# Kernel optimization log

Hardware: AMD Instinct MI355X
Metric: run time of the kernel (lower is better)

The kernel has to match this reference:

```python
import math
import numpy as np
import jax
import jax.numpy as jnp

B_IN, B_L1, B_L2 = 10, 6, 3
BATCH, NUM_POINTS = 4, 512
F1, F2, F_OUT = 8, 16, 10
NB = BATCH * NUM_POINTS
N_GRID_S2, N_GRID_SO3 = 24, 144


def _lf(n):
    return math.lgamma(n + 1)


def wigner_d(l, beta):
    """Wigner small-d matrices d^l_{m',m}(beta). beta: np [K] -> [K, 2l+1, 2l+1]."""
    beta = np.asarray(beta, dtype=np.float64)
    K = beta.shape[0]
    d = np.zeros((K, 2 * l + 1, 2 * l + 1))
    c, s = np.cos(beta / 2.0), np.sin(beta / 2.0)
    for mi, mp in enumerate(range(-l, l + 1)):
        for ni, m in enumerate(range(-l, l + 1)):
            k0, k1 = max(0, m - mp), min(l + m, l - mp)
            acc = np.zeros(K)
            for k in range(k0, k1 + 1):
                lg = 0.5 * (_lf(l + mp) + _lf(l - mp) + _lf(l + m) + _lf(l - m)) - _lf(l + m - k) - _lf(k) - _lf(mp - m + k) - _lf(l - mp - k)
                acc = acc + ((-1.0) ** (mp - m + k)) * np.exp(lg) * c ** (2 * l - 2 * k + m - mp) * s ** (mp - m + 2 * k)
            d[:, mi, ni] = acc
    return d


def quad_beta_weights(b):
    """Driscoll-Healy quadrature betas and weights at bandwidth b."""
    k = np.arange(2 * b)
    beta = np.pi * (2 * k + 1) / (4 * b)
    j = np.arange(b)[:, None]
    w = (2.0 / b) * np.sin(beta) * np.sum(np.sin((2 * j + 1) * beta[None, :]) / (2 * j + 1), axis=0)
    return beta, w


# near-identity kernel grids (as in s2cnn): s2 grid 3 betas x 8 alphas, so3 grid x 6 gammas
_b = np.arange(1, 4) * (np.pi / 8) / 3
_a = np.linspace(0, 2 * np.pi, 8, endpoint=False)
_GB1, _GA1 = [g.ravel() for g in np.meshgrid(_b, _a, indexing='ij')]
_g = np.linspace(0, 2 * np.pi, 6, endpoint=False)
_GB2, _GA2, _GG2 = [g.ravel() for g in np.meshgrid(_b, _a, _g, indexing='ij')]

_BETA_IN, _W_IN = quad_beta_weights(B_IN)
_BETA_L1, _W_L1 = quad_beta_weights(B_L1)
_BETA_L2, _W_L2 = quad_beta_weights(B_L2)

# S2 FFT tables: quadrature-weighted d^l_{m,0}(beta_k), l < b_l1
_S2FFT_D = [jnp.asarray((wigner_d(l, _BETA_IN)[:, :, l] * _W_IN[:, None]).astype(np.complex64)) for l in range(B_L1)]
# S2 kernel basis psi1[l]: [24, 2l+1] = d^l_{m,0}(beta_g) e^{-i m alpha_g}
_PSI1 = []
for l in range(B_L1):
    m = np.arange(-l, l + 1)
    _PSI1.append(jnp.asarray((wigner_d(l, _GB1)[:, :, l] * np.exp(-1j * m[None, :] * _GA1[:, None])).astype(np.complex64)))
# SO3 inverse-FFT d matrices at b_l1 quadrature betas
_D_L1 = [jnp.asarray(wigner_d(l, _BETA_L1).astype(np.complex64)) for l in range(B_L1)]
# SO3 FFT tables at b_l1 (output bandwidth b_l2)
_SO3FFT_D = [jnp.asarray((wigner_d(l, _BETA_L1) * _W_L1[:, None, None]).astype(np.complex64)) for l in range(B_L2)]
# SO3 kernel basis psi2[l]: [144, 2l+1, 2l+1] = e^{-i m a} d^l_{mn}(b) e^{-i n g}
_PSI2 = []
for l in range(B_L2):
    m = np.arange(-l, l + 1)
    ph = np.exp(-1j * m[None, :, None] * _GA2[:, None, None]) * np.exp(-1j * m[None, None, :] * _GG2[:, None, None])
    _PSI2.append(jnp.asarray((wigner_d(l, _GB2) * ph).astype(np.complex64)))
_D_L2 = [jnp.asarray(wigner_d(l, _BETA_L2).astype(np.complex64)) for l in range(B_L2)]
_W_INT = jnp.asarray(_W_L2.astype(np.float32))


def s2_fft(x, b_out):
    # x: [n, f, 2b(beta), 2b(alpha)] real -> list_l of [n, f, 2l+1] complex
    two_b = x.shape[-1]
    F = jnp.fft.fft(x, axis=-1)
    out = []
    for l in range(b_out):
        idx = np.arange(-l, l + 1) % two_b
        out.append(jnp.einsum('nfkm,km->nfm', F[..., idx], _S2FFT_D[l]))
    return out


def so3_ifft_list(z, b_out, d_list):
    # z[l]: [n, fo, 2l+1(m), 2l+1(p)] -> real [n, fo, 2b(beta), 2b(alpha), 2b(gamma)]
    n2 = 2 * b_out
    n, fo = z[0].shape[:2]
    Fh = jnp.zeros((n, fo, n2, n2, n2), jnp.complex64)
    for l in range(b_out):
        idx = np.arange(-l, l + 1) % n2
        blk = (2 * l + 1) * jnp.einsum('nomp,kmp->nokmp', z[l], d_list[l])
        Fh = Fh.at[:, :, :, idx[:, None], idx[None, :]].add(blk)
    return jnp.real(jnp.fft.ifft2(Fh, axes=(-2, -1)) * (n2 * n2))


def s2_conv(x, w, bias):
    xs = s2_fft(x, B_L1)
    wc = w.astype(jnp.complex64)
    z = []
    for l in range(B_L1):
        y = jnp.einsum('iog,gm->iom', wc, _PSI1[l])  # kernel spectrum [fi, fo, 2l+1]
        z.append(jnp.einsum('nim,iop->nomp', xs[l], jnp.conj(y)))
    return so3_ifft_list(z, B_L1, _D_L1) + bias[None, :, None, None, None]


def so3_fft(x, b_out):
    # x: [n, f, 2b(beta), 2b(alpha), 2b(gamma)] -> list_l of [n, f, 2l+1, 2l+1]
    two_b = x.shape[-1]
    F = jnp.fft.fft2(x, axes=(-2, -1))
    out = []
    for l in range(b_out):
        idx = np.arange(-l, l + 1) % two_b
        out.append(jnp.einsum('nfkmp,kmp->nfmp', F[:, :, :, idx[:, None], idx[None, :]], _SO3FFT_D[l]))
    return out


def so3_conv(x, w, bias):
    xs = so3_fft(x, B_L2)
    wc = w.astype(jnp.complex64)
    z = []
    for l in range(B_L2):
        y = jnp.einsum('iog,gmp->iomp', wc, _PSI2[l])  # [fi, fo, 2l+1, 2l+1]
        z.append(jnp.einsum('nimk,iopk->nomp', xs[l], jnp.conj(y)))
    return so3_ifft_list(z, B_L2, _D_L2) + bias[None, :, None, None, None]


def so3_integrate(x):
    # mean over alpha, gamma; quadrature-weighted sum over beta
    return jnp.einsum('nfk,k->nf', x.mean(axis=(-2, -1)), _W_INT)


def forward(x, w1, b1, w2, b2, w_out, bias_out):
    h = jax.nn.relu(s2_conv(x, w1, b1))
    h = jax.nn.relu(so3_conv(h, w2, b2))
    feat = so3_integrate(h).reshape(BATCH, NUM_POINTS, F2).transpose(0, 2, 1)  # [B, F2, P]
    pooled = feat.max(axis=-1)  # MaxPool1d(kernel_size=num_points) + squeeze
    return pooled @ w_out.T + bias_out


def setup_inputs():
    ks = jax.random.split(jax.random.key(0), 4)
    return {
        'x': jax.random.normal(ks[0], (NB, 1, 2 * B_IN, 2 * B_IN), jnp.float32),
        'w1': jax.random.normal(ks[1], (1, F1, N_GRID_S2), jnp.float32) * 0.1,
        'b1': jnp.zeros((F1,), jnp.float32),
        'w2': jax.random.normal(ks[2], (F1, F2, N_GRID_SO3), jnp.float32) * 0.05,
        'b2': jnp.zeros((F2,), jnp.float32),
        'w_out': jax.random.normal(ks[3], (F_OUT, F2), jnp.float32) * 0.1,
        'bias_out': jnp.zeros((F_OUT,), jnp.float32),
    }


def reference(x, w1, b1, w2, b2, w_out, bias_out):
    return forward(x, w1, b1, w2, b2, w_out, bias_out)
```

## Files before the change

### kernel.cpp

```cpp
#include <hip/hip_runtime.h>
#include <cmath>

typedef float2 c32;

__device__ __forceinline__ void cmadd(c32& acc, c32 a, float cr, float ci){
    acc.x += a.x*cr - a.y*ci;
    acc.y += a.x*ci + a.y*cr;
}

__host__ __device__ constexpr int M12(int x){ return ((x%12)+12)%12; }
__host__ __device__ constexpr int M6(int x){ return ((x%6)+6)%6; }

#define SQ32 0.86602540378443864676f
#define RT22 0.70710678118654752440f
static constexpr float CW12[12] = {1.f, SQ32, 0.5f, 0.f, -0.5f, -SQ32, -1.f, -SQ32, -0.5f, 0.f, 0.5f, SQ32};
static constexpr float SW12[12] = {0.f, 0.5f, SQ32, 1.f, SQ32, 0.5f, 0.f, -0.5f, -SQ32, -1.f, -SQ32, -0.5f};
static constexpr float CW6[6] = {1.f, 0.5f, -0.5f, -1.f, -0.5f, 0.5f};
static constexpr float SW6[6] = {0.f, SQ32, SQ32, 0.f, -SQ32, -SQ32};
static constexpr float CW8[8] = {1.f, RT22, 0.f, -RT22, -1.f, -RT22, 0.f, RT22};
static constexpr float SW8[8] = {0.f, RT22, 1.f, RT22, 0.f, -RT22, -1.f, -RT22};
static constexpr float CW20_[6] = {1.f, 0.95105651629515357212f, 0.80901699437494742410f,
                                   0.58778525229247312917f, 0.30901699437494742410f, 0.f};
static constexpr float SW20_[6] = {0.f, 0.30901699437494742410f, 0.58778525229247312917f,
                                   0.80901699437494742410f, 0.95105651629515357212f, 1.f};

#define O_CY1  0
#define O_CY2P 528
#define O_XS   (O_CY2P + 14080)
#define O_XS2P (O_XS + 73728)
#define N_C32_TOTAL (O_XS2P + 2048*8*30)

#define O_S2D  0
#define O_D1S  1752
#define O_DG   (O_D1S + 6336)
#define O_D2P  (O_DG + 360)
#define O_POOLP (O_D2P + 360)

#define DPI 3.14159265358979323846

__device__ __forceinline__ void cell_decode(int c, int& L, int& m, int& p){
    int base;
    if (c < 1){ L=0; base=0; } else if (c < 6){ L=1; base=1; }
    else if (c < 15){ L=2; base=6; } else if (c < 28){ L=3; base=15; }
    else if (c < 45){ L=4; base=28; } else { L=5; base=45; }
    int r = c - base;
    if (r < 2*L){ m = r>>1; p = (r&1)? L : -L; }
    else { m = L; p = (r - 2*L) - L; }
}

static constexpr double FCT[13] = {1.,1.,2.,6.,24.,120.,720.,5040.,40320.,
                                   362880.,3628800.,39916800.,479001600.};

__device__ __forceinline__ double dipow(double b, int e){
    double r = 1.0;
    while (e){ if (e & 1) r *= b; b *= b; e >>= 1; }
    return r;
}

__device__ double dev_wig(int l, int mp, int m, double beta){
    int k0 = max(0, m - mp), k1 = min(l + m, l - mp);
    double c = cos(0.5*beta), s = sin(0.5*beta);
    double fnum = sqrt(FCT[l+mp]*FCT[l-mp]*FCT[l+m]*FCT[l-m]);
    double acc = 0.0;
    for (int k = k0; k <= k1; ++k){
        double t = fnum / (FCT[l+m-k]*FCT[k]*FCT[mp-m+k]*FCT[l-mp-k])
                 * dipow(c, 2*l-2*k+m-mp) * dipow(s, mp-m+2*k);
        acc += ((mp-m+k) & 1) ? -t : t;
    }
    return acc;
}

__device__ double dev_qw(int b, double beta){
    double s = 0.0;
    for (int j = 0; j < b; ++j) s += sin((2.0*j+1.0)*beta)/(2.0*j+1.0);
    return (2.0/b)*sin(beta)*s;
}

__global__ __launch_bounds__(256) void k_setup(c32* cb, float* fb,
                                               const float* __restrict__ w1,
                                               const float* __restrict__ w2){
    __shared__ float wsh[144];
    __shared__ float s_d2sg[225];
    __shared__ c32 W1s[3][8][5];
    __shared__ c32 Rs[3][5][5];
    int bid = blockIdx.x, tid = threadIdx.x;
    if (bid < 128){
        int o = bid >> 3, i = bid & 7;
        for (int c = tid; c < 144; c += 256) wsh[c] = w2[(i*16+o)*144 + c];
        for (int c = tid; c < 225; c += 256){
            int qi = c%5; int t = c/5; int pi = t%5; t /= 5; int ib = t%3; int l = t/3;
            float v = 0.f;
            if (pi < 2*l+1 && qi < 2*l+1){ double beta = (ib+1)*DPI/24.0; v = (float)dev_wig(l, pi-l, qi-l, beta); }
            s_d2sg[c] = v;
        }
        __syncthreads();
        for (int c = tid; c < 120; c += 256){
            int ib = c/40, r = c%40, ia = r/5, qi = r%5;
            int q = qi - 2; int qm = ((q%6)+6)%6;
            float wr = CW6[qm], wi = SW6[qm];
            float er = 1.f, ei = 0.f, sx = 0.f, sy = 0.f;
            const float* wrow = wsh + ib*48 + ia*6;
            #pragma unroll
            for (int ig = 0; ig < 6; ++ig){
                float w = wrow[ig];
                sx += w*er; sy += w*ei;
                float nr = er*wr - ei*wi; ei = er*wi + ei*wr; er = nr;
            }
            W1s[ib][ia][qi] = make_float2(sx, sy);
        }
        __syncthreads();
        for (int c = tid; c < 75; c += 256){
            int ib = c/25, r = c%25, pi = r/5, qi = r%5;
            int p = pi - 2; int pm = ((p%8)+8)%8;
            float wr = CW8[pm], wi = SW8[pm];
            float er = 1.f, ei = 0.f;
            c32 acc = make_float2(0.f,0.f);
            #pragma unroll
            for (int ia = 0; ia < 8; ++ia){
                c32 wv = W1s[ib][ia][qi];
                acc.x += wv.x*er - wv.y*ei;
                acc.y += wv.x*ei + wv.y*er;
                float nr = er*wr - ei*wi; ei = er*wi + ei*wr; er = nr;
            }
            Rs[ib][pi][qi] = acc;
        }
        __syncthreads();
        for (int c = tid; c < 110; c += 256){
            int cell = c/5, qt = c%5;
            int l, p;
            if (cell == 0){ l=0; p=0; }
            else if (cell < 7){ l=1; p=(cell-1)%3 - 1; }
            else { l=2; p=(cell-7)%5 - 2; }
            c32 acc = make_float2(0.f,0.f);
            if (qt < 2*l+1){
                int q = qt - l;
                #pragma unroll
                for (int ib = 0; ib < 3; ++ib){
                    float d = s_d2sg[(l*3+ib)*25 + (p+l)*5 + (q+l)];
                    c32 rv = Rs[ib][p+2][q+2];
                    acc.x += d*rv.x; acc.y += d*rv.y;
                }
            }
            cb[O_CY2P + ((o*22+cell)*8 + i)*5 + qt] = acc;
        }
        return;
    }
    int gid = (bid-128)*256 + tid;
    if (gid < 1320){
        int mi = gid%11; int t = gid/11; int k = t%20; int l = t/20;
        float v = 0.f;
        if (mi < 2*l+1){
            double beta = DPI*(2*k+1)/40.0;
            v = (float)(dev_wig(l, mi-l, 0, beta) * dev_qw(10, beta));
        }
        fb[O_S2D+gid] = v; return;
    }
    gid -= 1320;
    if (gid < 528){
        int pi = gid%11; int t = gid/11; int l = t%6; int o = t/6;
        c32 acc = make_float2(0.f,0.f);
        if (pi < 2*l+1){
            int p = pi - l;
            int pm = ((p%8)+8)%8;
            float wr = CW8[pm], wi = SW8[pm];
            for (int ib = 0; ib < 3; ++ib){
                float d = (float)dev_wig(l, pi-l, 0, (ib+1)*DPI/24.0);
                float er = 1.f, ei = 0.f, sx = 0.f, sy = 0.f;
                #pragma unroll
                for (int ia = 0; ia < 8; ++ia){
                    float w = w1[o*24 + ib*8 + ia];
                    sx += w*er; sy += w*ei;
                    float nr = er*wr - ei*wi; ei = er*wi + ei*wr; er = nr;
                }
                acc.x += d*sx; acc.y += d*sy;
            }
        }
        cb[O_CY1 + (o*6+l)*11 + pi] = acc;
        return;
    }
    gid -= 528;
    if (gid < 6336){
        int k = gid%12; int t = gid/12; int l = t%8; int cell = t/8;
        int L, m, p; cell_decode(cell, L, m, p);
        float v = 0.f;
        if (l < 6 && l >= L){
            double beta = DPI*(2*k+1)/24.0;
            v = (float)dev_wig(l, m, p, beta);
        }
        fb[O_D1S+gid] = v; return;
    }
    gid -= 6336;
    if (gid < 360){
        int k = gid%12; int slot = gid/12;
        int lm = slot/5, qt = slot%5;
        int l = lm==0?0:(lm<3?1:2);
        int m = lm==0?0:(lm<3?lm-1:lm-3);
        float v = 0.f;
        if (qt < 2*l+1){
            double beta = DPI*(2*k+1)/24.0;
            v = (float)(dev_wig(l, m, qt-l, beta) * dev_qw(6, beta));
        }
        fb[O_DG+gid] = v; return;
    }
    gid -= 360;
    if (gid < 360){
        int lp = gid%4; int t = gid/4; int k = t%6; int cell = t/6;
        int m = cell/5, pi = cell%5, p = pi-2, ap = p<0?-p:p;
        float v = 0.f;
        if (lp < 3 && lp >= m && lp >= ap){
            double beta = DPI*(2*k+1)/12.0;
            v = (float)dev_wig(lp, m, p, beta);
        }
        fb[O_D2P+gid] = v; return;
    }
}

__global__ __launch_bounds__(256) void k_s2fft(const float* __restrict__ x, const float* __restrict__ fb,
                                               c32* __restrict__ XS){
    __shared__ float xsh[1600];
    __shared__ c32 F1[4][20][6];
    int n0 = blockIdx.x*4, tid = threadIdx.x;
    for (int i = tid; i < 1600; i += 256) xsh[i] = x[n0*400 + i];
    __syncthreads();
    for (int i = tid; i < 480; i += 256){
        int nl = i/120, r = i - nl*120, k = r/6, m = r - k*6;
        float wr = CW20_[m], wi = -SW20_[m];
        float er = 1.f, ei = 0.f, ax = 0.f, ay = 0.f;
        const float* row = xsh + nl*400 + k*20;
        #pragma unroll
        for (int a = 0; a < 20; ++a){
            float v = row[a];
            ax += v*er; ay += v*ei;
            float nr = er*wr - ei*wi; ei = er*wi + ei*wr; er = nr;
        }
        F1[nl][k][m] = make_float2(ax, ay);
    }
    __syncthreads();
    if (tid < 144){
        int nl = tid/36, t = tid - nl*36;
        int l = 0; while ((l+1)*(l+1) <= t) ++l;
        int mi = t - l*l; int m = mi - l;
        c32 acc = make_float2(0.f,0.f);
        for (int k = 0; k < 20; ++k){
            float d = fb[O_S2D + (l*20+k)*11 + mi];
            c32 F = (m >= 0) ? F1[nl][k][m] : make_float2(F1[nl][k][-m].x, -F1[nl][k][-m].y);
            acc.x += d*F.x; acc.y += d*F.y;
        }
        XS[(n0+nl)*36 + t] = acc;
    }
}

__global__ __launch_bounds__(256) void k_layer1(const c32* __restrict__ cb, const float* __restrict__ fb,
                                                const float* __restrict__ b1, c32* __restrict__ xs2p){
    __shared__ c32 xs_sh[36];
    __shared__ c32 u1[936];
    __shared__ c32 u2[936];
    __shared__ c32 Gg[468];
    __shared__ c32 Gs[180];
    int tid = threadIdx.x;
    int n = blockIdx.x >> 3, o = blockIdx.x & 7;
    float bias = b1[o];
    if (tid < 36) xs_sh[tid] = cb[O_XS + n*36 + tid];
    __syncthreads();

    for (int c = tid; c < 396; c += 256){
        int l = c/66, mp = c - l*66, m = mp/11, pi = mp - m*11;
        int p = pi - 5, ap = p < 0 ? -p : p;
        c32 v = make_float2(0.f, 0.f);
        if (m <= l && ap <= l){
            c32 a = xs_sh[l*l + l + m];
            c32 b = cb[O_CY1 + o*66 + l*11 + p + l];
            float f = (float)(2*l+1);
            v.x = f*(a.x*b.x - a.y*b.y); v.y = f*(a.x*b.y + a.y*b.x);
        }
        u1[c] = v;
    }
    __syncthreads();

    if (tid < 132){
        int cell = tid >> 1, kh = tid & 1;
        int L, m, p; cell_decode(cell, L, m, p);
        int mp = m*11 + p + 5;
        c32 acc[6];
        #pragma unroll
        for (int j = 0; j < 6; ++j) acc[j] = make_float2(0.f,0.f);
        for (int l = L; l < 6; ++l){
            c32 z = u1[l*66 + mp];
            const float* dp = fb + O_D1S + (cell*8 + l)*12 + kh*6;
            #pragma unroll
            for (int j = 0; j < 6; ++j){
                float d = dp[j];
                acc[j].x += d*z.x; acc[j].y += d*z.y;
            }
        }
        #pragma unroll
        for (int j = 0; j < 6; ++j) u2[mp*13 + kh*6 + j] = acc[j];
    }
    __syncthreads();

    if (tid < 72){
        int m = tid/12, k = tid - m*12;
        c32 S0 = u2[(m*11+5)*13 + k];
        c32 E[5], O[5];
        #pragma unroll
        for (int p = 1; p <= 5; ++p){
            c32 a = u2[(m*11+5+p)*13 + k], b = u2[(m*11+5-p)*13 + k];
            E[p-1] = make_float2(a.x+b.x, a.y+b.y);
            O[p-1] = make_float2(a.x-b.x, a.y-b.y);
        }
        #pragma unroll
        for (int g = 0; g < 6; ++g){
            float vex=0.f, vey=0.f, vox=0.f, voy=0.f;
            #pragma unroll
            for (int p = 1; p <= 5; ++p){
                const float cc = CW12[M12(p*g)], ss = SW12[M12(p*g)];
                float vx = E[p-1].x*cc - O[p-1].y*ss;
                float vy = E[p-1].y*cc + O[p-1].x*ss;
                if (p & 1){ vox += vx; voy += vy; } else { vex += vx; vey += vy; }
            }
            float tex = S0.x + vex, tey = S0.y + vey;
            u1[(m*12+g)*13 + k]   = make_float2(tex + vox, tey + voy);
            u1[(m*12+g+6)*13 + k] = make_float2(tex - vox, tey - voy);
        }
    }
    __syncthreads();

    float* hh = (float*)u2;
    if (tid < 144){
        int g = tid/12, k = tid - g*12;
        c32 t1 = u1[(1*12+g)*13+k], t2 = u1[(2*12+g)*13+k], t3 = u1[(3*12+g)*13+k];
        c32 t4 = u1[(4*12+g)*13+k], t5 = u1[(5*12+g)*13+k];
        float base = u1[(0*12+g)*13+k].x + bias;
        #pragma unroll
        for (int a = 0; a < 6; ++a){
            float od = t1.x*CW12[M12(1*a)] - t1.y*SW12[M12(1*a)]
                     + t3.x*CW12[M12(3*a)] - t3.y*SW12[M12(3*a)]
                     + t5.x*CW12[M12(5*a)] - t5.y*SW12[M12(5*a)];
            float ev = t2.x*CW12[M12(2*a)] - t2.y*SW12[M12(2*a)]
                     + t4.x*CW12[M12(4*a)] - t4.y*SW12[M12(4*a)];
            float h0 = base + 2.f*(ev+od);
            float h1 = base + 2.f*(ev-od);
            hh[(g*12+a)*13+k]     = h0 > 0.f ? h0 : 0.f;
            hh[(g*12+a+6)*13+k]   = h1 > 0.f ? h1 : 0.f;
        }
    }
    __syncthreads();

    if (tid < 144){
        int a = tid/12, k = tid - a*12;
        float hv[12];
        #pragma unroll
        for (int g = 0; g < 12; ++g) hv[g] = hh[(g*12+a)*13+k];
        float s0 = 0.f;
        #pragma unroll
        for (int g = 0; g < 12; ++g) s0 += hv[g];
        Gg[a*13+k] = make_float2(s0, 0.f);
        #pragma unroll
        for (int mg = 1; mg < 3; ++mg){
            float ax = 0.f, ay = 0.f;
            #pragma unroll
            for (int g = 0; g < 12; ++g){
                const int tt = M12(mg*g);
                ax += hv[g]*CW12[tt]; ay -= hv[g]*SW12[tt];
            }
            Gg[(mg*12+a)*13+k] = make_float2(ax, ay);
        }
    }
    __syncthreads();

    if (tid < 108){
        int j = tid/36, rr = tid - j*36, mg = rr/12, k = rr - mg*12;
        const c32* gp = Gg + mg*156 + k;
        if (j == 0){
            float sx = 0.f, sy = 0.f;
            #pragma unroll
            for (int a = 0; a < 6; ++a){
                c32 xa = gp[a*13], ya = gp[(a+6)*13];
                sx += xa.x + ya.x; sy += xa.y + ya.y;
            }
            Gs[(2*3+mg)*12+k] = make_float2(sx, sy);
        } else if (j == 1){
            float Cx=0.f,Cy=0.f,Sx=0.f,Sy=0.f;
            #pragma unroll
            for (int a = 0; a < 6; ++a){
                c32 xa = gp[a*13], ya = gp[(a+6)*13];
                float ux = xa.x - ya.x, uy = xa.y - ya.y;
                const float cc = CW12[a], ss = SW12[a];
                Cx += ux*cc; Cy += uy*cc;
                Sx += ux*ss; Sy += uy*ss;
            }
            Gs[(3*3+mg)*12+k] = make_float2(Cx + Sy, Cy - Sx);
            Gs[(1*3+mg)*12+k] = make_float2(Cx - Sy, Cy + Sx);
        } else {
            float Cx=0.f,Cy=0.f,Sx=0.f,Sy=0.f;
            #pragma unroll
            for (int a = 0; a < 6; ++a){
                c32 xa = gp[a*13], ya = gp[(a+6)*13];
                float ux = xa.x + ya.x, uy = xa.y + ya.y;
                const float cc = CW12[M12(2*a)], ss = SW12[M12(2*a)];
                Cx += ux*cc; Cy += uy*cc;
                Sx += ux*ss; Sy += uy*ss;
            }
            Gs[(4*3+mg)*12+k] = make_float2(Cx + Sy, Cy - Sx);
            Gs[(0*3+mg)*12+k] = make_float2(Cx - Sy, Cy + Sx);
        }
    }
    __syncthreads();

    if (tid < 30){
        int lm = tid/5, qt = tid - lm*5;
        int l = lm==0?0:(lm<3?1:2);
        int m = lm==0?0:(lm<3?lm-1:lm-3);
        c32 acc = make_float2(0.f,0.f);
        if (qt < 2*l+1){
            int q = qt - l;
            #pragma unroll
            for (int k = 0; k < 12; ++k){
                float d = fb[O_DG + tid*12 + k];
                c32 gvv;
                if (q >= 0) gvv = Gs[((m+2)*3 + q)*12 + k];
                else { c32 w = Gs[((2-m)*3 + (-q))*12 + k]; gvv = make_float2(w.x, -w.y); }
                acc.x += d*gvv.x; acc.y += d*gvv.y;
            }
        }
        xs2p[(n*8+o)*30 + tid] = acc;
    }
}

__global__ __launch_bounds__(256) void k_layer2(const c32* __restrict__ cb, const float* __restrict__ fb,
                                                const float* __restrict__ b2, float* __restrict__ poolp){
    __shared__ c32 xs2sh[960];
    __shared__ c32 zp2[4][384];
    __shared__ c32 T2[1728];
    __shared__ float part[576];
    __shared__ float wint_sh[6];
    int tid = threadIdx.x, n0 = blockIdx.x*4;
    for (int c = tid; c < 960; c += 256) xs2sh[c] = cb[O_XS2P + n0*240 + c];
    if (tid < 6){ double beta = DPI*(2*tid+1)/12.0; wint_sh[tid] = (float)dev_qw(3, beta); }
    __syncthreads();

    for (int c = tid; c < 352; c += 256){
        int o = c/22, cell = c - o*22;
        int l, lm;
        if (cell == 0){ l=0; lm=0; }
        else if (cell < 7){ l=1; lm=1+(cell-1)/3; }
        else { l=2; lm=3+(cell-7)/5; }
        const c32* cy = cb + O_CY2P + (o*22+cell)*40;
        c32 acc[4];
        #pragma unroll
        for (int nl = 0; nl < 4; ++nl) acc[nl] = make_float2(0.f,0.f);
        #pragma unroll
        for (int i = 0; i < 8; ++i){
            #pragma unroll
            for (int qt = 0; qt < 5; ++qt){
                c32 yv = cy[i*5+qt];
                #pragma unroll
                for (int nl = 0; nl < 4; ++nl){
                    c32 xv = xs2sh[nl*240 + (i*6+lm)*5 + qt];
                    acc[nl].x += xv.x*yv.x - xv.y*yv.y;
                    acc[nl].y += xv.x*yv.y + xv.y*yv.x;
                }
            }
        }
        float f = (float)(2*l+1);
        #pragma unroll
        for (int nl = 0; nl < 4; ++nl)
            zp2[nl][o*24+cell] = make_float2(f*acc[nl].x, f*acc[nl].y);
    }
    __syncthreads();

    float runmax = -3.4e38f;
    for (int nl = 0; nl < 4; ++nl){
        for (int c = tid; c < 288; c += 256){
            int o = c/18, r = c - o*18, k = r/3, m = r - k*3;
            c32 s2v[5];
            #pragma unroll
            for (int pi = 0; pi < 5; ++pi){
                const int p = pi-2; const int ap = p<0?-p:p;
                c32 acc = make_float2(0.f,0.f);
                #pragma unroll
                for (int l = 0; l < 3; ++l){
                    if (l >= ap){
                        float d = fb[O_D2P + ((m*5+pi)*6+k)*4 + l];
                        int cell = (l==0) ? 0 : ((l==1) ? 1+m*3+(p+1) : 7+m*5+(p+2));
                        c32 z = zp2[nl][o*24+cell];
                        acc.x += d*z.x; acc.y += d*z.y;
                    }
                }
                s2v[pi] = acc;
            }
            #pragma unroll
            for (int g = 0; g < 6; ++g){
                c32 t = make_float2(0.f,0.f);
                #pragma unroll
                for (int pi = 0; pi < 5; ++pi){
                    const int tt = M6((pi-2)*g);
                    cmadd(t, s2v[pi], CW6[tt], SW6[tt]);
                }
                T2[((o*6+k)*3+m)*6+g] = t;
            }
        }
        __syncthreads();
        for (int c = tid; c < 576; c += 256){
            int o = c/36, r = c - o*36, k = r/6, g = r - k*6;
            c32 t0 = T2[((o*6+k)*3+0)*6+g];
            c32 t1 = T2[((o*6+k)*3+1)*6+g];
            c32 t2 = T2[((o*6+k)*3+2)*6+g];
            float base = t0.x + b2[o];
            float s = 0.f;
            #pragma unroll
            for (int a = 0; a < 6; ++a){
                float h = base + 2.f*(t1.x*CW6[M6(a)]   - t1.y*SW6[M6(a)])
                               + 2.f*(t2.x*CW6[M6(2*a)] - t2.y*SW6[M6(2*a)]);
                s += h > 0.f ? h : 0.f;
            }
            part[c] = s * wint_sh[k];
        }
        __syncthreads();
        if (tid < 16){
            float s = 0.f;
            #pragma unroll
            for (int j = 0; j < 36; ++j) s += part[tid*36+j];
            runmax = fmaxf(runmax, s * (1.f/36.f));
        }
        __syncthreads();
    }
    if (tid < 16) poolp[blockIdx.x*16 + tid] = runmax;
}

__global__ __launch_bounds__(256) void k_head(const float* __restrict__ poolp,
                                              const float* __restrict__ w_out,
                                              const float* __restrict__ bias_out,
                                              float* __restrict__ out){
    __shared__ float red[256];
    __shared__ float pool_s[64];
    int tid = threadIdx.x;
    int pair = tid >> 2, q = tid & 3;
    int b = pair >> 4, o = pair & 15;
    float m = -3.4e38f;
    for (int j = q; j < 128; j += 4)
        m = fmaxf(m, poolp[(b*128 + j)*16 + o]);
    red[tid] = m;
    __syncthreads();
    if (tid < 64)
        pool_s[tid] = fmaxf(fmaxf(red[tid*4], red[tid*4+1]),
                            fmaxf(red[tid*4+2], red[tid*4+3]));
    __syncthreads();
    if (tid < 40){
        int bb = tid/10, jj = tid%10;
        float s = bias_out[jj];
        #pragma unroll
        for (int oo = 0; oo < 16; ++oo) s += pool_s[bb*16+oo]*w_out[jj*16+oo];
        out[tid] = s;
    }
}

extern "C" void kernel_launch(void* const* d_in, const int* in_sizes, int n_in,
                              void* d_out, int out_size, void* d_ws, size_t ws_size,
                              hipStream_t stream){
    const float* x        = (const float*)d_in[0];
    const float* w1       = (const float*)d_in[1];
    const float* b1       = (const float*)d_in[2];
    const float* w2       = (const float*)d_in[3];
    const float* b2       = (const float*)d_in[4];
    const float* w_out    = (const float*)d_in[5];
    const float* bias_out = (const float*)d_in[6];
    float* out = (float*)d_out;

    c32*   cb = (c32*)d_ws;
    float* fb = (float*)(cb + N_C32_TOTAL);

    k_setup<<<163, 256, 0, stream>>>(cb, fb, w1, w2);
    k_s2fft<<<512, 256, 0, stream>>>(x, fb, cb + O_XS);
    k_layer1<<<2048*8, 256, 0, stream>>>(cb, fb, b1, cb + O_XS2P);
    k_layer2<<<512, 256, 0, stream>>>(cb, fb, b2, fb + O_POOLP);
    k_head<<<1, 256, 0, stream>>>(fb + O_POOLP, w_out, bias_out, out);
}
```

Before: 172.9 us.

## Fuse all stages into one persistent cooperative kernel with grid syncs

Merges the S2 FFT, layer-1, layer-2 and head kernels into a single persistent cooperative kernel. Blocks loop over work units and use grid-wide syncs between stages, and shared memory is reused through one aliased buffer. Layer 2 now handles one point per unit instead of four, so the reuse of each CY2P load across points is lost. Per-point features are written out and then pooled in a final stage. The change removes launch overhead and inter-kernel gaps, at the cost of grid-sync overhead and occupancy limited to co-resident blocks.

```diff
diff --git a/kernel.cpp b/kernel.cpp
--- a/kernel.cpp
+++ b/kernel.cpp
@@ -1,5 +1,8 @@
 #include <hip/hip_runtime.h>
+#include <hip/hip_cooperative_groups.h>
 #include <cmath>
+
+namespace cg = cooperative_groups;
 
 typedef float2 c32;
 
@@ -34,7 +37,8 @@
 #define O_D1S  1752
 #define O_DG   (O_D1S + 6336)
 #define O_D2P  (O_DG + 360)
-#define O_POOLP (O_D2P + 360)
+#define O_WINT (O_D2P + 360)
+#define O_FEAT (O_WINT + 8)
 
 #define DPI 3.14159265358979323846
 
@@ -213,345 +217,358 @@
         }
         fb[O_D2P+gid] = v; return;
     }
-}
-
-__global__ __launch_bounds__(256) void k_s2fft(const float* __restrict__ x, const float* __restrict__ fb,
-                                               c32* __restrict__ XS){
-    __shared__ float xsh[1600];
-    __shared__ c32 F1[4][20][6];
-    int n0 = blockIdx.x*4, tid = threadIdx.x;
-    for (int i = tid; i < 1600; i += 256) xsh[i] = x[n0*400 + i];
-    __syncthreads();
-    for (int i = tid; i < 480; i += 256){
-        int nl = i/120, r = i - nl*120, k = r/6, m = r - k*6;
-        float wr = CW20_[m], wi = -SW20_[m];
-        float er = 1.f, ei = 0.f, ax = 0.f, ay = 0.f;
-        const float* row = xsh + nl*400 + k*20;
-        #pragma unroll
-        for (int a = 0; a < 20; ++a){
-            float v = row[a];
-            ax += v*er; ay += v*ei;
-            float nr = er*wr - ei*wi; ei = er*wi + ei*wr; er = nr;
-        }
-        F1[nl][k][m] = make_float2(ax, ay);
-    }
-    __syncthreads();
-    if (tid < 144){
-        int nl = tid/36, t = tid - nl*36;
-        int l = 0; while ((l+1)*(l+1) <= t) ++l;
-        int mi = t - l*l; int m = mi - l;
-        c32 acc = make_float2(0.f,0.f);
-        for (int k = 0; k < 20; ++k){
-            float d = fb[O_S2D + (l*20+k)*11 + mi];
-            c32 F = (m >= 0) ? F1[nl][k][m] : make_float2(F1[nl][k][-m].x, -F1[nl][k][-m].y);
-            acc.x += d*F.x; acc.y += d*F.y;
-        }
-        XS[(n0+nl)*36 + t] = acc;
-    }
-}
-
-__global__ __launch_bounds__(256) void k_layer1(const c32* __restrict__ cb, const float* __restrict__ fb,
-                                                const float* __restrict__ b1, c32* __restrict__ xs2p){
-    __shared__ c32 xs_sh[36];
-    __shared__ c32 u1[936];
-    __shared__ c32 u2[936];
-    __shared__ c32 Gg[468];
-    __shared__ c32 Gs[180];
+    gid -= 360;
+    if (gid < 6){
+        double beta = DPI*(2*gid+1)/12.0;
+        fb[O_WINT+gid] = (float)dev_qw(3, beta); return;
+    }
+}
+
+__global__ __launch_bounds__(256) void k_fused(const float* __restrict__ x,
+                                               c32* __restrict__ cb,
+                                               const float* __restrict__ fb,
+                                               const float* __restrict__ b1,
+                                               const float* __restrict__ b2,
+                                               const float* __restrict__ w_out,
+                                               const float* __restrict__ bias_out,
+                                               float* __restrict__ feat,
+                                               float* __restrict__ out){
+    __shared__ c32 U[2556];
+    cg::grid_group grid = cg::this_grid();
     int tid = threadIdx.x;
-    int n = blockIdx.x >> 3, o = blockIdx.x & 7;
-    float bias = b1[o];
-    if (tid < 36) xs_sh[tid] = cb[O_XS + n*36 + tid];
-    __syncthreads();
-
-    for (int c = tid; c < 396; c += 256){
-        int l = c/66, mp = c - l*66, m = mp/11, pi = mp - m*11;
-        int p = pi - 5, ap = p < 0 ? -p : p;
-        c32 v = make_float2(0.f, 0.f);
-        if (m <= l && ap <= l){
-            c32 a = xs_sh[l*l + l + m];
-            c32 b = cb[O_CY1 + o*66 + l*11 + p + l];
-            float f = (float)(2*l+1);
-            v.x = f*(a.x*b.x - a.y*b.y); v.y = f*(a.x*b.y + a.y*b.x);
-        }
-        u1[c] = v;
-    }
-    __syncthreads();
-
-    if (tid < 132){
-        int cell = tid >> 1, kh = tid & 1;
-        int L, m, p; cell_decode(cell, L, m, p);
-        int mp = m*11 + p + 5;
-        c32 acc[6];
-        #pragma unroll
-        for (int j = 0; j < 6; ++j) acc[j] = make_float2(0.f,0.f);
-        for (int l = L; l < 6; ++l){
-            c32 z = u1[l*66 + mp];
-            const float* dp = fb + O_D1S + (cell*8 + l)*12 + kh*6;
+    int nblk = gridDim.x;
+
+    {
+        float* xsh = (float*)U;
+        c32* F1 = U + 800;
+        for (int u = blockIdx.x; u < 512; u += nblk){
+            int n0 = u*4;
+            for (int i = tid; i < 1600; i += 256) xsh[i] = x[n0*400 + i];
+            __syncthreads();
+            for (int i = tid; i < 480; i += 256){
+                int nl = i/120, r = i - nl*120, k = r/6, m = r - k*6;
+                float wr = CW20_[m], wi = -SW20_[m];
+                float er = 1.f, ei = 0.f, ax = 0.f, ay = 0.f;
+                const float* row = xsh + nl*400 + k*20;
+                #pragma unroll
+                for (int a = 0; a < 20; ++a){
+                    float v = row[a];
+                    ax += v*er; ay += v*ei;
+                    float nr = er*wr - ei*wi; ei = er*wi + ei*wr; er = nr;
+                }
+                F1[(nl*20+k)*6+m] = make_float2(ax, ay);
+            }
+            __syncthreads();
+            if (tid < 144){
+                int nl = tid/36, t = tid - nl*36;
+                int l = 0; while ((l+1)*(l+1) <= t) ++l;
+                int mi = t - l*l; int m = mi - l;
+                c32 acc = make_float2(0.f,0.f);
+                for (int k = 0; k < 20; ++k){
+                    float d = fb[O_S2D + (l*20+k)*11 + mi];
+                    c32 F = (m >= 0) ? F1[(nl*20+k)*6+m]
+                                     : make_float2(F1[(nl*20+k)*6-m].x, -F1[(nl*20+k)*6-m].y);
+                    acc.x += d*F.x; acc.y += d*F.y;
+                }
+                cb[O_XS + (n0+nl)*36 + t] = acc;
+            }
+            __syncthreads();
+        }
+    }
+    grid.sync();
+
+    {
+        c32* u1 = U;
+        c32* u2 = U + 936;
+        c32* Gg = U + 1872;
+        c32* Gs = U + 2340;
+        c32* xs_sh = U + 2520;
+        float* hh = (float*)u2;
+        for (int u = blockIdx.x; u < 16384; u += nblk){
+            int n = u >> 3, o = u & 7;
+            float bias = b1[o];
+            if (tid < 36) xs_sh[tid] = cb[O_XS + n*36 + tid];
+            __syncthreads();
+
+            for (int c = tid; c < 396; c += 256){
+                int l = c/66, mp = c - l*66, m = mp/11, pi = mp - m*11;
+                int p = pi - 5, ap = p < 0 ? -p : p;
+                c32 v = make_float2(0.f, 0.f);
+                if (m <= l && ap <= l){
+                    c32 a = xs_sh[l*l + l + m];
+                    c32 b = cb[O_CY1 + o*66 + l*11 + p + l];
+                    float f = (float)(2*l+1);
+                    v.x = f*(a.x*b.x - a.y*b.y); v.y = f*(a.x*b.y + a.y*b.x);
+                }
+                u1[c] = v;
+            }
+            __syncthreads();
+
+            if (tid < 132){
+                int cell = tid >> 1, kh = tid & 1;
+                int L, m, p; cell_decode(cell, L, m, p);
+                int mp = m*11 + p + 5;
+                c32 acc[6];
+                #pragma unroll
+                for (int j = 0; j < 6; ++j) acc[j] = make_float2(0.f,0.f);
+                for (int l = L; l < 6; ++l){
+                    c32 z = u1[l*66 + mp];
+                    const float* dp = fb + O_D1S + (cell*8 + l)*12 + kh*6;
+                    #pragma unroll
+                    for (int j = 0; j < 6; ++j){
+                        float d = dp[j];
+                        acc[j].x += d*z.x; acc[j].y += d*z.y;
+                    }
+                }
+                #pragma unroll
+                for (int j = 0; j < 6; ++j) u2[mp*13 + kh*6 + j] = acc[j];
+            }
+            __syncthreads();
+
+            if (tid < 72){
+                int m = tid/12, k = tid - m*12;
+                c32 S0 = u2[(m*11+5)*13 + k];
+                c32 E[5], O[5];
+                #pragma unroll
+                for (int p = 1; p <= 5; ++p){
+                    c32 a = u2[(m*11+5+p)*13 + k], b = u2[(m*11+5-p)*13 + k];
+                    E[p-1] = make_float2(a.x+b.x, a.y+b.y);
+                    O[p-1] = make_float2(a.x-b.x, a.y-b.y);
+                }
+                #pragma unroll
+                for (int g = 0; g < 6; ++g){
+                    float vex=0.f, vey=0.f, vox=0.f, voy=0.f;
+                    #pragma unroll
+                    for (int p = 1; p <= 5; ++p){
+                        const float cc = CW12[M12(p*g)], ss = SW12[M12(p*g)];
+                        float vx = E[p-1].x*cc - O[p-1].y*ss;
+                        float vy = E[p-1].y*cc + O[p-1].x*ss;
+                        if (p & 1){ vox += vx; voy += vy; } else { vex += vx; vey += vy; }
+                    }
+                    float tex = S0.x + vex, tey = S0.y + vey;
+                    u1[(m*12+g)*13 + k]   = make_float2(tex + vox, tey + voy);
+                    u1[(m*12+g+6)*13 + k] = make_float2(tex - vox, tey - voy);
+                }
+            }
+            __syncthreads();
+
+            if (tid < 144){
+                int g = tid/12, k = tid - g*12;
+                c32 t1 = u1[(1*12+g)*13+k], t2 = u1[(2*12+g)*13+k], t3 = u1[(3*12+g)*13+k];
+                c32 t4 = u1[(4*12+g)*13+k], t5 = u1[(5*12+g)*13+k];
+                float base = u1[(0*12+g)*13+k].x + bias;
+                #pragma unroll
+                for (int a = 0; a < 6; ++a){
+                    float od = t1.x*CW12[M12(1*a)] - t1.y*SW12[M12(1*a)]
+                             + t3.x*CW12[M12(3*a)] - t3.y*SW12[M12(3*a)]
+                             + t5.x*CW12[M12(5*a)] - t5.y*SW12[M12(5*a)];
+                    float ev = t2.x*CW12[M12(2*a)] - t2.y*SW12[M12(2*a)]
+                             + t4.x*CW12[M12(4*a)] - t4.y*SW12[M12(4*a)];
+                    float h0 = base + 2.f*(ev+od);
+                    float h1 = base + 2.f*(ev-od);
+                    hh[(g*12+a)*13+k]     = h0 > 0.f ? h0 : 0.f;
+                    hh[(g*12+a+6)*13+k]   = h1 > 0.f ? h1 : 0.f;
+                }
+            }
+            __syncthreads();
+
+            if (tid < 144){
+                int a = tid/12, k = tid - a*12;
+                float hv[12];
+                #pragma unroll
+                for (int g = 0; g < 12; ++g) hv[g] = hh[(g*12+a)*13+k];
+                float s0 = 0.f;
+                #pragma unroll
+                for (int g = 0; g < 12; ++g) s0 += hv[g];
+                Gg[a*13+k] = make_float2(s0, 0.f);
+                #pragma unroll
+                for (int mg = 1; mg < 3; ++mg){
+                    float ax = 0.f, ay = 0.f;
+                    #pragma unroll
+                    for (int g = 0; g < 12; ++g){
+                        const int tt = M12(mg*g);
+                        ax += hv[g]*CW12[tt]; ay -= hv[g]*SW12[tt];
+                    }
+                    Gg[(mg*12+a)*13+k] = make_float2(ax, ay);
+                }
+            }
+            __syncthreads();
+
+            if (tid < 108){
+                int j = tid/36, rr = tid - j*36, mg = rr/12, k = rr - mg*12;
+                const c32* gp = Gg + mg*156 + k;
+                if (j == 0){
+                    float sx = 0.f, sy = 0.f;
+                    #pragma unroll
+                    for (int a = 0; a < 6; ++a){
+                        c32 xa = gp[a*13], ya = gp[(a+6)*13];
+                        sx += xa.x + ya.x; sy += xa.y + ya.y;
+                    }
+                    Gs[(2*3+mg)*12+k] = make_float2(sx, sy);
+                } else if (j == 1){
+                    float Cx=0.f,Cy=0.f,Sx=0.f,Sy=0.f;
+                    #pragma unroll
+                    for (int a = 0; a < 6; ++a){
+                        c32 xa = gp[a*13], ya = gp[(a+6)*13];
+                        float ux = xa.x - ya.x, uy = xa.y - ya.y;
+                        const float cc = CW12[a], ss = SW12[a];
+                        Cx += ux*cc; Cy += uy*cc;
+                        Sx += ux*ss; Sy += uy*ss;
+                    }
+                    Gs[(3*3+mg)*12+k] = make_float2(Cx + Sy, Cy - Sx);
+                    Gs[(1*3+mg)*12+k] = make_float2(Cx - Sy, Cy + Sx);
+                } else {
+                    float Cx=0.f,Cy=0.f,Sx=0.f,Sy=0.f;
+                    #pragma unroll
+                    for (int a = 0; a < 6; ++a){
+                        c32 xa = gp[a*13], ya = gp[(a+6)*13];
+                        float ux = xa.x + ya.x, uy = xa.y + ya.y;
+                        const float cc = CW12[M12(2*a)], ss = SW12[M12(2*a)];
+                        Cx += ux*cc; Cy += uy*cc;
+                        Sx += ux*ss; Sy += uy*ss;
+                    }
+                    Gs[(4*3+mg)*12+k] = make_float2(Cx + Sy, Cy - Sx);
+                    Gs[(0*3+mg)*12+k] = make_float2(Cx - Sy, Cy + Sx);
+                }
+            }
+            __syncthreads();
+
+            if (tid < 30){
+                int lm = tid/5, qt = tid - lm*5;
+                int l = lm==0?0:(lm<3?1:2);
+                int m = lm==0?0:(lm<3?lm-1:lm-3);
+                c32 acc = make_float2(0.f,0.f);
+                if (qt < 2*l+1){
+                    int q = qt - l;
+                    #pragma unroll
+                    for (int k = 0; k < 12; ++k){
+                        float d = fb[O_DG + tid*12 + k];
+                        c32 gvv;
+                        if (q >= 0) gvv = Gs[((m+2)*3 + q)*12 + k];
+                        else { c32 w = Gs[((2-m)*3 + (-q))*12 + k]; gvv = make_float2(w.x, -w.y); }
+                        acc.x += d*gvv.x; acc.y += d*gvv.y;
+                    }
+                }
+                cb[O_XS2P + (n*8+o)*30 + tid] = acc;
+            }
+            __syncthreads();
+        }
+    }
+    grid.sync();
+
+    {
+        c32* xs2sh = U;
+        c32* zp2   = U + 240;
+        c32* T2    = U + 624;
+        float* part = (float*)U;
+        float* wint_sh = (float*)(U + 2530);
+        for (int u = blockIdx.x; u < 2048; u += nblk){
+            if (tid < 240) xs2sh[tid] = cb[O_XS2P + u*240 + tid];
+            if (tid >= 248 && tid < 254) wint_sh[tid-248] = fb[O_WINT + tid-248];
+            __syncthreads();
+
+            for (int c = tid; c < 352; c += 256){
+                int o = c/22, cell = c - o*22;
+                int l, lm;
+                if (cell == 0){ l=0; lm=0; }
+                else if (cell < 7){ l=1; lm=1+(cell-1)/3; }
+                else { l=2; lm=3+(cell-7)/5; }
+                const c32* cy = cb + O_CY2P + (o*22+cell)*40;
+                c32 acc = make_float2(0.f,0.f);
+                #pragma unroll
+                for (int i = 0; i < 8; ++i){
+                    #pragma unroll
+                    for (int qt = 0; qt < 5; ++qt){
+                        c32 xv = xs2sh[(i*6+lm)*5 + qt];
+                        c32 yv = cy[i*5+qt];
+                        acc.x += xv.x*yv.x - xv.y*yv.y;
+                        acc.y += xv.x*yv.y + xv.y*yv.x;
+                    }
+                }
+                float f = (float)(2*l+1);
+                zp2[o*24+cell] = make_float2(f*acc.x, f*acc.y);
+            }
+            __syncthreads();
+
+            for (int c = tid; c < 288; c += 256){
+                int o = c/18, r = c - o*18, k = r/3, m = r - k*3;
+                c32 s2v[5];
+                #pragma unroll
+                for (int pi = 0; pi < 5; ++pi){
+                    const int p = pi-2; const int ap = p<0?-p:p;
+                    c32 acc = make_float2(0.f,0.f);
+                    #pragma unroll
+                    for (int l = 0; l < 3; ++l){
+                        if (l >= ap){
+                            float d = fb[O_D2P + ((m*5+pi)*6+k)*4 + l];
+                            int cell = (l==0) ? 0 : ((l==1) ? 1+m*3+(p+1) : 7+m*5+(p+2));
+                            c32 z = zp2[o*24+cell];
+                            acc.x += d*z.x; acc.y += d*z.y;
+                        }
+                    }
+                    s2v[pi] = acc;
+                }
+                #pragma unroll
+                for (int g = 0; g < 6; ++g){
+                    c32 t = make_float2(0.f,0.f);
+                    #pragma unroll
+                    for (int pi = 0; pi < 5; ++pi){
+                        const int tt = M6((pi-2)*g);
+                        cmadd(t, s2v[pi], CW6[tt], SW6[tt]);
+                    }
+                    T2[((o*6+k)*3+m)*6+g] = t;
+                }
+            }
+            __syncthreads();
+
+            for (int c = tid; c < 576; c += 256){
+                int o = c/36, r = c - o*36, k = r/6, g = r - k*6;
+                c32 t0 = T2[((o*6+k)*3+0)*6+g];
+                c32 t1 = T2[((o*6+k)*3+1)*6+g];
+                c32 t2 = T2[((o*6+k)*3+2)*6+g];
+                float base = t0.x + b2[o];
+                float s = 0.f;
+                #pragma unroll
+                for (int a = 0; a < 6; ++a){
+                    float h = base + 2.f*(t1.x*CW6[M6(a)]   - t1.y*SW6[M6(a)])
+                                   + 2.f*(t2.x*CW6[M6(2*a)] - t2.y*SW6[M6(2*a)]);
+                    s += h > 0.f ? h : 0.f;
+                }
+                part[c] = s * wint_sh[k];
+            }
+            __syncthreads();
+            if (tid < 16){
+                float s = 0.f;
+                #pragma unroll
+                for (int j = 0; j < 36; ++j) s += part[tid*36+j];
+                feat[u*16+tid] = s * (1.f/36.f);
+            }
+            __syncthreads();
+        }
+    }
+    grid.sync();
+
+    if (blockIdx.x == 0){
+        float* red = (float*)U;
+        float* pool_s = (float*)(U + 128);
+        int pair = tid >> 2, q = tid & 3;
+        int b = pair >> 4, o = pair & 15;
+        float m = -3.4e38f;
+        for (int j = q; j < 512; j += 4)
+            m = fmaxf(m, feat[(b*512+j)*16 + o]);
+        red[tid] = m;
+        __syncthreads();
+        if (tid < 64)
+            pool_s[tid] = fmaxf(fmaxf(red[tid*4], red[tid*4+1]),
+                                fmaxf(red[tid*4+2], red[tid*4+3]));
+        __syncthreads();
+        if (tid < 40){
+            int bb = tid/10, jj = tid%10;
+            float s = bias_out[jj];
             #pragma unroll
-            for (int j = 0; j < 6; ++j){
-                float d = dp[j];
-                acc[j].x += d*z.x; acc[j].y += d*z.y;
-            }
-        }
-        #pragma unroll
-        for (int j = 0; j < 6; ++j) u2[mp*13 + kh*6 + j] = acc[j];
-    }
-    __syncthreads();
-
-    if (tid < 72){
-        int m = tid/12, k = tid - m*12;
-        c32 S0 = u2[(m*11+5)*13 + k];
-        c32 E[5], O[5];
-        #pragma unroll
-        for (int p = 1; p <= 5; ++p){
-            c32 a = u2[(m*11+5+p)*13 + k], b = u2[(m*11+5-p)*13 + k];
-            E[p-1] = make_float2(a.x+b.x, a.y+b.y);
-            O[p-1] = make_float2(a.x-b.x, a.y-b.y);
-        }
-        #pragma unroll
-        for (int g = 0; g < 6; ++g){
-            float vex=0.f, vey=0.f, vox=0.f, voy=0.f;
-            #pragma unroll
-            for (int p = 1; p <= 5; ++p){
-                const float cc = CW12[M12(p*g)], ss = SW12[M12(p*g)];
-                float vx = E[p-1].x*cc - O[p-1].y*ss;
-                float vy = E[p-1].y*cc + O[p-1].x*ss;
-                if (p & 1){ vox += vx; voy += vy; } else { vex += vx; vey += vy; }
-            }
-            float tex = S0.x + vex, tey = S0.y + vey;
-            u1[(m*12+g)*13 + k]   = make_float2(tex + vox, tey + voy);
-            u1[(m*12+g+6)*13 + k] = make_float2(tex - vox, tey - voy);
-        }
-    }
-    __syncthreads();
-
-    float* hh = (float*)u2;
-    if (tid < 144){
-        int g = tid/12, k = tid - g*12;
-        c32 t1 = u1[(1*12+g)*13+k], t2 = u1[(2*12+g)*13+k], t3 = u1[(3*12+g)*13+k];
-        c32 t4 = u1[(4*12+g)*13+k], t5 = u1[(5*12+g)*13+k];
-        float base = u1[(0*12+g)*13+k].x + bias;
-        #pragma unroll
-        for (int a = 0; a < 6; ++a){
-            float od = t1.x*CW12[M12(1*a)] - t1.y*SW12[M12(1*a)]
-                     + t3.x*CW12[M12(3*a)] - t3.y*SW12[M12(3*a)]
-                     + t5.x*CW12[M12(5*a)] - t5.y*SW12[M12(5*a)];
-            float ev = t2.x*CW12[M12(2*a)] - t2.y*SW12[M12(2*a)]
-                     + t4.x*CW12[M12(4*a)] - t4.y*SW12[M12(4*a)];
-            float h0 = base + 2.f*(ev+od);
-            float h1 = base + 2.f*(ev-od);
-            hh[(g*12+a)*13+k]     = h0 > 0.f ? h0 : 0.f;
-            hh[(g*12+a+6)*13+k]   = h1 > 0.f ? h1 : 0.f;
-        }
-    }
-    __syncthreads();
-
-    if (tid < 144){
-        int a = tid/12, k = tid - a*12;
-        float hv[12];
-        #pragma unroll
-        for (int g = 0; g < 12; ++g) hv[g] = hh[(g*12+a)*13+k];
-        float s0 = 0.f;
-        #pragma unroll
-        for (int g = 0; g < 12; ++g) s0 += hv[g];
-        Gg[a*13+k] = make_float2(s0, 0.f);
-        #pragma unroll
-        for (int mg = 1; mg < 3; ++mg){
-            float ax = 0.f, ay = 0.f;
-            #pragma unroll
-            for (int g = 0; g < 12; ++g){
-                const int tt = M12(mg*g);
-                ax += hv[g]*CW12[tt]; ay -= hv[g]*SW12[tt];
-            }
-            Gg[(mg*12+a)*13+k] = make_float2(ax, ay);
-        }
-    }
-    __syncthreads();
-
-    if (tid < 108){
-        int j = tid/36, rr = tid - j*36, mg = rr/12, k = rr - mg*12;
-        const c32* gp = Gg + mg*156 + k;
-        if (j == 0){
-            float sx = 0.f, sy = 0.f;
-            #pragma unroll
-            for (int a = 0; a < 6; ++a){
-                c32 xa = gp[a*13], ya = gp[(a+6)*13];
-                sx += xa.x + ya.x; sy += xa.y + ya.y;
-            }
-            Gs[(2*3+mg)*12+k] = make_float2(sx, sy);
-        } else if (j == 1){
-            float Cx=0.f,Cy=0.f,Sx=0.f,Sy=0.f;
-            #pragma unroll
-            for (int a = 0; a < 6; ++a){
-                c32 xa = gp[a*13], ya = gp[(a+6)*13];
-                float ux = xa.x - ya.x, uy = xa.y - ya.y;
-                const float cc = CW12[a], ss = SW12[a];
-                Cx += ux*cc; Cy += uy*cc;
-                Sx += ux*ss; Sy += uy*ss;
-            }
-            Gs[(3*3+mg)*12+k] = make_float2(Cx + Sy, Cy - Sx);
-            Gs[(1*3+mg)*12+k] = make_float2(Cx - Sy, Cy + Sx);
-        } else {
-            float Cx=0.f,Cy=0.f,Sx=0.f,Sy=0.f;
-            #pragma unroll
-            for (int a = 0; a < 6; ++a){
-                c32 xa = gp[a*13], ya = gp[(a+6)*13];
-                float ux = xa.x + ya.x, uy = xa.y + ya.y;
-                const float cc = CW12[M12(2*a)], ss = SW12[M12(2*a)];
-                Cx += ux*cc; Cy += uy*cc;
-                Sx += ux*ss; Sy += uy*ss;
-            }
-            Gs[(4*3+mg)*12+k] = make_float2(Cx + Sy, Cy - Sx);
-            Gs[(0*3+mg)*12+k] = make_float2(Cx - Sy, Cy + Sx);
-        }
-    }
-    __syncthreads();
-
-    if (tid < 30){
-        int lm = tid/5, qt = tid - lm*5;
-        int l = lm==0?0:(lm<3?1:2);
-        int m = lm==0?0:(lm<3?lm-1:lm-3);
-        c32 acc = make_float2(0.f,0.f);
-        if (qt < 2*l+1){
-            int q = qt - l;
-            #pragma unroll
-            for (int k = 0; k < 12; ++k){
-                float d = fb[O_DG + tid*12 + k];
-                c32 gvv;
-                if (q >= 0) gvv = Gs[((m+2)*3 + q)*12 + k];
-                else { c32 w = Gs[((2-m)*3 + (-q))*12 + k]; gvv = make_float2(w.x, -w.y); }
-                acc.x += d*gvv.x; acc.y += d*gvv.y;
-            }
-        }
-        xs2p[(n*8+o)*30 + tid] = acc;
-    }
-}
-
-__global__ __launch_bounds__(256) void k_layer2(const c32* __restrict__ cb, const float* __restrict__ fb,
-                                                const float* __restrict__ b2, float* __restrict__ poolp){
-    __shared__ c32 xs2sh[960];
-    __shared__ c32 zp2[4][384];
-    __shared__ c32 T2[1728];
-    __shared__ float part[576];
-    __shared__ float wint_sh[6];
-    int tid = threadIdx.x, n0 = blockIdx.x*4;
-    for (int c = tid; c < 960; c += 256) xs2sh[c] = cb[O_XS2P + n0*240 + c];
-    if (tid < 6){ double beta = DPI*(2*tid+1)/12.0; wint_sh[tid] = (float)dev_qw(3, beta); }
-    __syncthreads();
-
-    for (int c = tid; c < 352; c += 256){
-        int o = c/22, cell = c - o*22;
-        int l, lm;
-        if (cell == 0){ l=0; lm=0; }
-        else if (cell < 7){ l=1; lm=1+(cell-1)/3; }
-        else { l=2; lm=3+(cell-7)/5; }
-        const c32* cy = cb + O_CY2P + (o*22+cell)*40;
-        c32 acc[4];
-        #pragma unroll
-        for (int nl = 0; nl < 4; ++nl) acc[nl] = make_float2(0.f,0.f);
-        #pragma unroll
-        for (int i = 0; i < 8; ++i){
-            #pragma unroll
-            for (int qt = 0; qt < 5; ++qt){
-                c32 yv = cy[i*5+qt];
-                #pragma unroll
-                for (int nl = 0; nl < 4; ++nl){
-                    c32 xv = xs2sh[nl*240 + (i*6+lm)*5 + qt];
-                    acc[nl].x += xv.x*yv.x - xv.y*yv.y;
-                    acc[nl].y += xv.x*yv.y + xv.y*yv.x;
-                }
-            }
-        }
-        float f = (float)(2*l+1);
-        #pragma unroll
-        for (int nl = 0; nl < 4; ++nl)
-            zp2[nl][o*24+cell] = make_float2(f*acc[nl].x, f*acc[nl].y);
-    }
-    __syncthreads();
-
-    float runmax = -3.4e38f;
-    for (int nl = 0; nl < 4; ++nl){
-        for (int c = tid; c < 288; c += 256){
-            int o = c/18, r = c - o*18, k = r/3, m = r - k*3;
-            c32 s2v[5];
-            #pragma unroll
-            for (int pi = 0; pi < 5; ++pi){
-                const int p = pi-2; const int ap = p<0?-p:p;
-                c32 acc = make_float2(0.f,0.f);
-                #pragma unroll
-                for (int l = 0; l < 3; ++l){
-                    if (l >= ap){
-                        float d = fb[O_D2P + ((m*5+pi)*6+k)*4 + l];
-                        int cell = (l==0) ? 0 : ((l==1) ? 1+m*3+(p+1) : 7+m*5+(p+2));
-                        c32 z = zp2[nl][o*24+cell];
-                        acc.x += d*z.x; acc.y += d*z.y;
-                    }
-                }
-                s2v[pi] = acc;
-            }
-            #pragma unroll
-            for (int g = 0; g < 6; ++g){
-                c32 t = make_float2(0.f,0.f);
-                #pragma unroll
-                for (int pi = 0; pi < 5; ++pi){
-                    const int tt = M6((pi-2)*g);
-                    cmadd(t, s2v[pi], CW6[tt], SW6[tt]);
-                }
-                T2[((o*6+k)*3+m)*6+g] = t;
-            }
-        }
-        __syncthreads();
-        for (int c = tid; c < 576; c += 256){
-            int o = c/36, r = c - o*36, k = r/6, g = r - k*6;
-            c32 t0 = T2[((o*6+k)*3+0)*6+g];
-            c32 t1 = T2[((o*6+k)*3+1)*6+g];
-            c32 t2 = T2[((o*6+k)*3+2)*6+g];
-            float base = t0.x + b2[o];
-            float s = 0.f;
-            #pragma unroll
-            for (int a = 0; a < 6; ++a){
-                float h = base + 2.f*(t1.x*CW6[M6(a)]   - t1.y*SW6[M6(a)])
-                               + 2.f*(t2.x*CW6[M6(2*a)] - t2.y*SW6[M6(2*a)]);
-                s += h > 0.f ? h : 0.f;
-            }
-            part[c] = s * wint_sh[k];
-        }
-        __syncthreads();
-        if (tid < 16){
-            float s = 0.f;
-            #pragma unroll
-            for (int j = 0; j < 36; ++j) s += part[tid*36+j];
-            runmax = fmaxf(runmax, s * (1.f/36.f));
-        }
-        __syncthreads();
-    }
-    if (tid < 16) poolp[blockIdx.x*16 + tid] = runmax;
-}
-
-__global__ __launch_bounds__(256) void k_head(const float* __restrict__ poolp,
-                                              const float* __restrict__ w_out,
-                                              const float* __restrict__ bias_out,
-                                              float* __restrict__ out){
-    __shared__ float red[256];
-    __shared__ float pool_s[64];
-    int tid = threadIdx.x;
-    int pair = tid >> 2, q = tid & 3;
-    int b = pair >> 4, o = pair & 15;
-    float m = -3.4e38f;
-    for (int j = q; j < 128; j += 4)
-        m = fmaxf(m, poolp[(b*128 + j)*16 + o]);
-    red[tid] = m;
-    __syncthreads();
-    if (tid < 64)
-        pool_s[tid] = fmaxf(fmaxf(red[tid*4], red[tid*4+1]),
-                            fmaxf(red[tid*4+2], red[tid*4+3]));
-    __syncthreads();
-    if (tid < 40){
-        int bb = tid/10, jj = tid%10;
-        float s = bias_out[jj];
-        #pragma unroll
-        for (int oo = 0; oo < 16; ++oo) s += pool_s[bb*16+oo]*w_out[jj*16+oo];
-        out[tid] = s;
+            for (int oo = 0; oo < 16; ++oo) s += pool_s[bb*16+oo]*w_out[jj*16+oo];
+            out[tid] = s;
+        }
     }
 }
 
@@ -569,10 +586,17 @@
 
     c32*   cb = (c32*)d_ws;
     float* fb = (float*)(cb + N_C32_TOTAL);
+    float* feat = fb + O_FEAT;
 
     k_setup<<<163, 256, 0, stream>>>(cb, fb, w1, w2);
-    k_s2fft<<<512, 256, 0, stream>>>(x, fb, cb + O_XS);
-    k_layer1<<<2048*8, 256, 0, stream>>>(cb, fb, b1, cb + O_XS2P);
-    k_layer2<<<512, 256, 0, stream>>>(cb, fb, b2, fb + O_POOLP);
-    k_head<<<1, 256, 0, stream>>>(fb + O_POOLP, w_out, bias_out, out);
-}
+
+    int nbPerCU = 0;
+    if (hipOccupancyMaxActiveBlocksPerMultiprocessor(&nbPerCU, k_fused, 256, 0) != hipSuccess || nbPerCU < 1)
+        nbPerCU = 4;
+    int grid = nbPerCU * 256;
+    if (grid > 2048) grid = 2048;
+
+    void* args[] = {(void*)&x, (void*)&cb, (void*)&fb, (void*)&b1, (void*)&b2,
+                    (void*)&w_out, (void*)&bias_out, (void*)&feat, (void*)&out};
+    hipLaunchCooperativeKernel((const void*)k_fused, dim3(grid), dim3(256), args, 0, stream);
+}
```

New measurement: 475.1 us. 175% more time.
